# Optimization experiments

Measured on AMD Instinct MI355X. Metric: run time of the kernel, lower is better.

Reference implementation:

```python
import jax, jax.numpy as jnp
import numpy as np

B, S, D, F, A, H, O = 8, 2048, 64, 16, 32, 4, 64
HD = A // H  # head dim = 8
TWO_PI = 2.0 * np.pi


def setup_inputs() -> dict:
    key = jax.random.key(0)
    ks = jax.random.split(key, 10)
    sc = lambda k, sh, fan: (jax.random.normal(k, sh, jnp.float32) / np.sqrt(fan)).astype(jnp.float32)
    Din = D + 2 * D * F  # input width to gate/projection MLPs
    return dict(
        x=jax.random.normal(ks[0], (B, S, D), jnp.float32),
        freq_matrix=jnp.tile(jnp.linspace(1.0, 10.0, F, dtype=jnp.float32)[None, :], (D, 1)),
        phase=jax.random.normal(ks[1], (D, F), jnp.float32),
        freq_scale=jnp.ones((D, F), jnp.float32),
        Wq=sc(ks[2], (A, D), D), bq=jnp.zeros((A,), jnp.float32),          # query_proj
        Wk1=sc(ks[3], (A, 1), 1), bk1=jnp.zeros((A,), jnp.float32),        # key_proj (Linear(1, A))
        Wqi=sc(ks[4], (A, A), A), bqi=jnp.zeros((A,), jnp.float32),        # MHA in-proj (q slice)
        Wki=sc(ks[5], (A, A), A), bki=jnp.zeros((A,), jnp.float32),        # MHA in-proj (k slice)
        Wg=sc(ks[6], (O, Din), Din), bg=jnp.zeros((O,), jnp.float32),      # gate linear
        Wp=sc(ks[7], (O, Din), Din), bp=jnp.zeros((O,), jnp.float32),      # projection linear
    )


def reference(x, freq_matrix, phase, freq_scale, Wq, bq, Wk1, bk1, Wqi, bqi, Wki, bki, Wg, bg, Wp, bp):
    # x: [B, S, D]
    t = jnp.linspace(0.0, 1.0, S, dtype=x.dtype)                 # [S]
    f = freq_matrix * freq_scale                                 # [D, F]
    # fourier signal, batched over all input dims at once
    signal = TWO_PI * t[:, None, None] * f[None] + phase[None]   # [S, D, F]
    sin_f, cos_f = jnp.sin(signal), jnp.cos(signal)

    # MHA attention weights (averaged over heads) -- attn_out is discarded by the module
    queries = jnp.einsum('bsd,ad->bsa', x, Wq) + bq              # [B, S, A]
    q = (jnp.einsum('bsa,ea->bse', queries, Wqi) + bqi).reshape(B, S, H, HD)
    keys = f[:, :, None] * Wk1[None, None, :, 0] + bk1           # [D, F, A] via Linear(1, A)
    k = (jnp.einsum('dfa,ea->dfe', keys, Wki) + bki).reshape(D, F, H, HD)
    scores = jnp.einsum('bshe,dfhe->bdhsf', q, k) / np.sqrt(HD)  # [B, D, H, S, F]
    attn = jax.nn.softmax(scores, axis=-1).mean(axis=2)          # [B, D, S, F] (head-avg)
    aw = jnp.transpose(attn, (0, 2, 1, 3))                       # [B, S, D, F]

    # weighted fourier features; per-dim layout is [sin(F), cos(F)] to match torch cat order
    ff = jnp.concatenate([sin_f[None] * aw, cos_f[None] * aw], axis=-1)  # [B, S, D, 2F]
    ff = ff.reshape(B, S, D * 2 * F)

    ci = jnp.concatenate([x, ff], axis=-1)                       # [B, S, D + 2DF]
    gated = jax.nn.sigmoid(jnp.einsum('bsi,oi->bso', ci, Wg) + bg) * \
            jax.nn.silu(jnp.einsum('bsi,oi->bso', ci, Wp) + bp)
    return x + gated
```

## Files before the change

kernel.cpp:

```cpp
#include <hip/hip_runtime.h>
#include <math.h>

#define SS 2048
#define DIN 2112
#define NKT 66
#define TOK 32
#define NBLK 512
#define NTHR 512
#define ASTR 264
#define XSTR 68
#define CSTR 132
#define BFRAG_ELEMS (NKT * 8 * 64 * 8)
#define LOG2E 1.4426950408889634f
#define INV2PI 0.15915494309189535f

#define OFF_WP 135168
#define OFF_CP 135424
#define OFF_FV 135680
#define OFF_PH 136704
#define OFF_MX 137728

typedef __attribute__((ext_vector_type(4))) float f32x4;
typedef __attribute__((ext_vector_type(8))) short bf16x8;

__device__ __forceinline__ unsigned short f2bf(float x) {
    union { float f; unsigned u; } v; v.f = x;
    unsigned r = v.u + 0x7FFFu + ((v.u >> 16) & 1u);
    return (unsigned short)(r >> 16);
}
__device__ __forceinline__ unsigned pk2bf(float a, float b) {
    union { float f; unsigned u; } ua, ub; ua.f = a; ub.f = b;
    unsigned ra = ua.u + 0x7FFFu + ((ua.u >> 16) & 1u);
    unsigned rb = ub.u + 0x7FFFu + ((ub.u >> 16) & 1u);
#if __has_builtin(__builtin_amdgcn_perm)
    return __builtin_amdgcn_perm(rb, ra, 0x07060302u);
#else
    return (ra >> 16) | (rb & 0xFFFF0000u);
#endif
}

#if __has_builtin(__builtin_amdgcn_exp2f)
#define EXP2(x) __builtin_amdgcn_exp2f(x)
#else
#define EXP2(x) exp2f(x)
#endif
#if __has_builtin(__builtin_amdgcn_rcpf)
#define RCP(x) __builtin_amdgcn_rcpf(x)
#else
#define RCP(x) (1.0f / (x))
#endif
#if __has_builtin(__builtin_amdgcn_sinf)
#define SINR(x) __builtin_amdgcn_sinf(x)
#define COSR(x) __builtin_amdgcn_cosf(x)
#else
#define SINR(x) __sinf(6.283185307179586f * (x))
#define COSR(x) __cosf(6.283185307179586f * (x))
#endif

__global__ __launch_bounds__(256) void aff_pre(
    const float* __restrict__ Wq, const float* __restrict__ bq,
    const float* __restrict__ Wk1,
    const float* __restrict__ Wqi, const float* __restrict__ bqi,
    const float* __restrict__ Wki,
    const float* __restrict__ Wg, const float* __restrict__ Wp,
    const float* __restrict__ fm, const float* __restrict__ fs,
    const float* __restrict__ phase,
    float* __restrict__ ws)
{
    unsigned short* Bf = (unsigned short*)ws;
    const int tid = threadIdx.x;
    const int gid = blockIdx.x * 256 + tid;

    {
        int j  = gid & 7;
        int q  = (gid >> 3) & 3;
        int nl = (gid >> 5) & 15;
        int nt = (gid >> 9) & 7;
        int kt = gid >> 12;
        int k = kt * 32 + q * 8 + j;
        int n = nt * 16 + nl;
        float s = (n < 64) ? Wg[(size_t)n * DIN + k] : Wp[(size_t)(n - 64) * DIN + k];
        int dst = ((kt * 8 + nt) * 64 + q * 16 + nl) * 8 + j;
        Bf[dst] = f2bf(s);
    }

    if (blockIdx.x == 0) {
        float* WP = ws + OFF_WP;
        float* cP = ws + OFF_CP;
        float* fvg = ws + OFF_FV;
        float* phg = ws + OFF_PH;
        float* mxg = ws + OFF_MX;

        {
            float4 a = ((const float4*)fm)[tid];
            float4 b = ((const float4*)fs)[tid];
            float4 r; r.x = a.x * b.x; r.y = a.y * b.y; r.z = a.z * b.z; r.w = a.w * b.w;
            ((float4*)fvg)[tid] = r;
            float4 p = ((const float4*)phase)[tid];
            p.x *= INV2PI; p.y *= INV2PI; p.z *= INV2PI; p.w *= INV2PI;
            ((float4*)phg)[tid] = p;
        }
        if (tid < 64) {
            float mx = -1e30f, mn = 1e30f;
            #pragma unroll
            for (int f = 0; f < 16; ++f) {
                float v = fm[tid * 16 + f] * fs[tid * 16 + f];
                mx = fmaxf(mx, v); mn = fminf(mn, v);
            }
            mxg[tid * 2] = mx; mxg[tid * 2 + 1] = mn;
        }

        __shared__ float u[32];
        if (tid < 32) {
            float s = 0.f;
            #pragma unroll
            for (int a = 0; a < 32; ++a) s += Wki[tid * 32 + a] * Wk1[a];
            u[tid] = s;
        }
        __syncthreads();
        {
            const int h = tid >> 6;
            const int d = tid & 63;
            float s = 0.f;
            for (int j = 0; j < 8; ++j) {
                int e = h * 8 + j;
                float wc = 0.f;
                #pragma unroll
                for (int a = 0; a < 32; ++a) wc += Wqi[e * 32 + a] * Wq[a * 64 + d];
                s += u[e] * wc;
            }
            WP[h * 64 + d] = s * 0.35355339059327373f * LOG2E;
            if (d == 0) {
                float sc = 0.f;
                for (int j = 0; j < 8; ++j) {
                    int e = h * 8 + j;
                    float bcv = bqi[e];
                    #pragma unroll
                    for (int a = 0; a < 32; ++a) bcv += Wqi[e * 32 + a] * bq[a];
                    sc += u[e] * bcv;
                }
                cP[h] = sc * 0.35355339059327373f * LOG2E;
            }
        }
    }
}

__global__ __launch_bounds__(NTHR, 6) void aff_main(
    const float* __restrict__ x,
    const float* __restrict__ ws_c,
    const float* __restrict__ bg, const float* __restrict__ bp,
    float* __restrict__ out)
{
    __shared__ __align__(16) float xs[TOK * XSTR];
    __shared__ __align__(16) unsigned short Ab[2][TOK * ASTR];
    __shared__ __align__(16) float Pl[TOK * 4];
    __shared__ __align__(16) float fvs[1024];
    __shared__ __align__(16) float phl[1024];
    __shared__ __align__(16) float mxs[128];

    const unsigned short* Bfu = (const unsigned short*)ws_c;
    const bf16x8* Bv = (const bf16x8*)Bfu;
    const float* WP  = ws_c + OFF_WP;
    const float* cP  = ws_c + OFF_CP;
    const float* fvg = ws_c + OFF_FV;
    const float* phg = ws_c + OFF_PH;
    const float* mxg = ws_c + OFF_MX;

    const int tid  = threadIdx.x;
    const int lane = tid & 63;
    const int w    = tid >> 6;
    const int t0   = blockIdx.x * TOK;
    const int lm   = lane & 15;
    const int lq   = lane >> 4;
    const int fh   = lq & 1;
    const int dsel = lane >> 5;
    const int dloc = ((w & 3) << 1) + dsel;
    const int tb   = ((w >> 2) << 4) + lm;

    if (tid < 256) {
        ((float4*)fvs)[tid] = ((const float4*)fvg)[tid];
        if (tid < 32) ((float4*)mxs)[tid] = ((const float4*)mxg)[tid];
    } else {
        ((float4*)phl)[tid - 256] = ((const float4*)phg)[tid - 256];
    }
    {
        int t = tid >> 4, j4 = (tid & 15) * 4;
        float4 xv = *(const float4*)(x + (size_t)(t0 + t) * 64 + j4);
        *(float4*)(xs + t * XSTR + j4) = xv;
    }
    __syncthreads();

    if (tid < 128) {
        int t = tid & 31, h = tid >> 5;
        float acc = cP[h];
        const float* wp = WP + h * 64;
        #pragma unroll 8
        for (int d = 0; d < 64; ++d) acc = fmaf(wp[d], xs[t * XSTR + d], acc);
        Pl[t * 4 + h] = acc;
    }

    f32x4 acc0 = {}, acc1 = {};

    #pragma unroll
    for (int ks = 0; ks < 2; ++ks) {
        bf16x8 b = Bv[((size_t)ks * 8 + w) * 64 + lane];
        #pragma unroll
        for (int mt = 0; mt < 2; ++mt) {
            const float* xr = xs + (mt * 16 + lm) * XSTR + ks * 32 + lq * 8;
            float4 fa = *(const float4*)xr;
            float4 fb = *(const float4*)(xr + 4);
            union { unsigned u[4]; bf16x8 v; } av;
            av.u[0] = pk2bf(fa.x, fa.y); av.u[1] = pk2bf(fa.z, fa.w);
            av.u[2] = pk2bf(fb.x, fb.y); av.u[3] = pk2bf(fb.z, fb.w);
            if (mt == 0) acc0 = __builtin_amdgcn_mfma_f32_16x16x32_bf16(av.v, b, acc0, 0, 0, 0);
            else         acc1 = __builtin_amdgcn_mfma_f32_16x16x32_bf16(av.v, b, acc1, 0, 0, 0);
        }
    }
    __syncthreads();

    const float w2 = (float)((t0 + tb) & (SS - 1)) * (1.0f / 2047.0f);

    auto build = [&](int ch, int buf) {
        const int d = ch * 8 + dloc;
        const float4 fA = *(const float4*)(fvs + d * 16 + fh * 8);
        const float4 fB = *(const float4*)(fvs + d * 16 + fh * 8 + 4);
        const float4 pA = *(const float4*)(phl + d * 16 + fh * 8);
        const float4 pB = *(const float4*)(phl + d * 16 + fh * 8 + 4);
        const float4 Pv = *(const float4*)(Pl + tb * 4);
        const float mxv = mxs[d * 2], mnv = mxs[d * 2 + 1];
        float fl[8] = {fA.x, fA.y, fA.z, fA.w, fB.x, fB.y, fB.z, fB.w};
        float pr[8] = {pA.x, pA.y, pA.z, pA.w, pB.x, pB.y, pB.z, pB.w};
        float aw[8] = {0.f, 0.f, 0.f, 0.f, 0.f, 0.f, 0.f, 0.f};
        float Ph4[4] = {Pv.x, Pv.y, Pv.z, Pv.w};
        #pragma unroll
        for (int h = 0; h < 4; ++h) {
            float Ph = Ph4[h];
            float m = fmaxf(mxv * Ph, mnv * Ph);
            float e[8]; float s = 0.f;
            #pragma unroll
            for (int j = 0; j < 8; ++j) { e[j] = EXP2(fmaf(fl[j], Ph, -m)); s += e[j]; }
            float z = s + __shfl_xor(s, 16);
            float inv = 0.25f * RCP(z);
            #pragma unroll
            for (int j = 0; j < 8; ++j) aw[j] = fmaf(e[j], inv, aw[j]);
        }
        unsigned sv[4], cv[4];
        #pragma unroll
        for (int jp = 0; jp < 4; ++jp) {
            int j0 = 2 * jp;
            float X0 = fmaf(w2, fl[j0], pr[j0]);
            float X1 = fmaf(w2, fl[j0 + 1], pr[j0 + 1]);
            float a0 = aw[j0], a1 = aw[j0 + 1];
            sv[jp] = pk2bf(a0 * SINR(X0), a1 * SINR(X1));
            cv[jp] = pk2bf(a0 * COSR(X0), a1 * COSR(X1));
        }
        unsigned short* dst = &Ab[buf][tb * ASTR + dloc * 32 + fh * 8];
        uint4 v0; v0.x = sv[0]; v0.y = sv[1]; v0.z = sv[2]; v0.w = sv[3];
        uint4 v1; v1.x = cv[0]; v1.y = cv[1]; v1.z = cv[2]; v1.w = cv[3];
        *(uint4*)dst = v0;
        *(uint4*)(dst + 16) = v1;
    };

    build(0, 0);
    __syncthreads();

    for (int ch = 0; ch < 8; ++ch) {
        const unsigned short* Ar = &Ab[ch & 1][0];
        #pragma unroll
        for (int ks = 0; ks < 8; ++ks) {
            const size_t kt = (size_t)(2 + ch * 8 + ks);
            bf16x8 b  = Bv[(kt * 8 + w) * 64 + lane];
            bf16x8 a0 = *(const bf16x8*)(Ar + lm * ASTR + ks * 32 + lq * 8);
            bf16x8 a1 = *(const bf16x8*)(Ar + (16 + lm) * ASTR + ks * 32 + lq * 8);
            acc0 = __builtin_amdgcn_mfma_f32_16x16x32_bf16(a0, b, acc0, 0, 0, 0);
            acc1 = __builtin_amdgcn_mfma_f32_16x16x32_bf16(a1, b, acc1, 0, 0, 0);
        }
        if (ch < 7) build(ch + 1, (ch + 1) & 1);
        __syncthreads();
    }

    float* Cb = (float*)(&Ab[0][0]);
    #pragma unroll
    for (int r = 0; r < 4; ++r) {
        Cb[(lq * 4 + r) * CSTR + w * 16 + lm]        = acc0[r];
        Cb[(16 + lq * 4 + r) * CSTR + w * 16 + lm]   = acc1[r];
    }
    __syncthreads();
    {
        int t = tid >> 4, o0 = (tid & 15) * 4;
        float4 g4 = *(float4*)(Cb + t * CSTR + o0);
        float4 p4 = *(float4*)(Cb + t * CSTR + 64 + o0);
        float4 bg4 = *(const float4*)(bg + o0);
        float4 bp4 = *(const float4*)(bp + o0);
        float4 xr = *(float4*)(xs + t * XSTR + o0);
        float4 o;
        { float g = g4.x + bg4.x, p = p4.x + bp4.x;
          float sg = RCP(1.f + EXP2(-g * LOG2E));
          float sp = RCP(1.f + EXP2(-p * LOG2E));
          o.x = fmaf(p * sg, sp, xr.x); }
        { float g = g4.y + bg4.y, p = p4.y + bp4.y;
          float sg = RCP(1.f + EXP2(-g * LOG2E));
          float sp = RCP(1.f + EXP2(-p * LOG2E));
          o.y = fmaf(p * sg, sp, xr.y); }
        { float g = g4.z + bg4.z, p = p4.z + bp4.z;
          float sg = RCP(1.f + EXP2(-g * LOG2E));
          float sp = RCP(1.f + EXP2(-p * LOG2E));
          o.z = fmaf(p * sg, sp, xr.z); }
        { float g = g4.w + bg4.w, p = p4.w + bp4.w;
          float sg = RCP(1.f + EXP2(-g * LOG2E));
          float sp = RCP(1.f + EXP2(-p * LOG2E));
          o.w = fmaf(p * sg, sp, xr.w); }
        *(float4*)(out + (size_t)(t0 + t) * 64 + o0) = o;
    }
}

extern "C" void kernel_launch(void* const* d_in, const int* in_sizes, int n_in,
                              void* d_out, int out_size, void* d_ws, size_t ws_size,
                              hipStream_t stream) {
    (void)in_sizes; (void)n_in; (void)out_size; (void)ws_size;
    const float* x    = (const float*)d_in[0];
    const float* fm   = (const float*)d_in[1];
    const float* phs  = (const float*)d_in[2];
    const float* fs   = (const float*)d_in[3];
    const float* Wq   = (const float*)d_in[4];
    const float* bq   = (const float*)d_in[5];
    const float* Wk1  = (const float*)d_in[6];
    const float* Wqi  = (const float*)d_in[8];
    const float* bqi  = (const float*)d_in[9];
    const float* Wki  = (const float*)d_in[10];
    const float* Wg   = (const float*)d_in[12];
    const float* bg   = (const float*)d_in[13];
    const float* Wp   = (const float*)d_in[14];
    const float* bp   = (const float*)d_in[15];
    float* out = (float*)d_out;
    float* ws  = (float*)d_ws;

    aff_pre<<<BFRAG_ELEMS / 256, 256, 0, stream>>>(Wq, bq, Wk1, Wqi, bqi, Wki, Wg, Wp,
                                                   fm, fs, phs, ws);
    aff_main<<<NBLK, NTHR, 0, stream>>>(x, (const float*)ws, bg, bp, out);
}
```

Measured before the change: 123.5 us.

## Halve token tile to 16 with 256 threads and switch MFMA operands to fp16

```diff
diff --git a/kernel.cpp b/kernel.cpp
--- a/kernel.cpp
+++ b/kernel.cpp
@@ -4,9 +4,9 @@
 #define SS 2048
 #define DIN 2112
 #define NKT 66
-#define TOK 32
-#define NBLK 512
-#define NTHR 512
+#define TOK 16
+#define NBLK 1024
+#define NTHR 256
 #define ASTR 264
 #define XSTR 68
 #define CSTR 132
@@ -21,21 +21,18 @@
 #define OFF_MX 137728
 
 typedef __attribute__((ext_vector_type(4))) float f32x4;
-typedef __attribute__((ext_vector_type(8))) short bf16x8;
-
-__device__ __forceinline__ unsigned short f2bf(float x) {
-    union { float f; unsigned u; } v; v.f = x;
-    unsigned r = v.u + 0x7FFFu + ((v.u >> 16) & 1u);
-    return (unsigned short)(r >> 16);
-}
-__device__ __forceinline__ unsigned pk2bf(float a, float b) {
-    union { float f; unsigned u; } ua, ub; ua.f = a; ub.f = b;
-    unsigned ra = ua.u + 0x7FFFu + ((ua.u >> 16) & 1u);
-    unsigned rb = ub.u + 0x7FFFu + ((ub.u >> 16) & 1u);
-#if __has_builtin(__builtin_amdgcn_perm)
-    return __builtin_amdgcn_perm(rb, ra, 0x07060302u);
+typedef __attribute__((ext_vector_type(8))) _Float16 f16x8;
+typedef __attribute__((ext_vector_type(2))) __fp16 fp16v2;
+
+__device__ __forceinline__ unsigned pkh(float a, float b) {
+#if __has_builtin(__builtin_amdgcn_cvt_pkrtz)
+    union { fp16v2 h; unsigned u; } r;
+    r.h = __builtin_amdgcn_cvt_pkrtz(a, b);
+    return r.u;
 #else
-    return (ra >> 16) | (rb & 0xFFFF0000u);
+    union { _Float16 h[2]; unsigned u; } r;
+    r.h[0] = (_Float16)a; r.h[1] = (_Float16)b;
+    return r.u;
 #endif
 }
 
@@ -67,7 +64,7 @@
     const float* __restrict__ phase,
     float* __restrict__ ws)
 {
-    unsigned short* Bf = (unsigned short*)ws;
+    _Float16* Bf = (_Float16*)ws;
     const int tid = threadIdx.x;
     const int gid = blockIdx.x * 256 + tid;
 
@@ -81,7 +78,7 @@
         int n = nt * 16 + nl;
         float s = (n < 64) ? Wg[(size_t)n * DIN + k] : Wp[(size_t)(n - 64) * DIN + k];
         int dst = ((kt * 8 + nt) * 64 + q * 16 + nl) * 8 + j;
-        Bf[dst] = f2bf(s);
+        Bf[dst] = (_Float16)s;
     }
 
     if (blockIdx.x == 0) {
@@ -145,21 +142,20 @@
     }
 }
 
-__global__ __launch_bounds__(NTHR, 6) void aff_main(
+__global__ __launch_bounds__(NTHR, 4) void aff_main(
     const float* __restrict__ x,
     const float* __restrict__ ws_c,
     const float* __restrict__ bg, const float* __restrict__ bp,
     float* __restrict__ out)
 {
     __shared__ __align__(16) float xs[TOK * XSTR];
-    __shared__ __align__(16) unsigned short Ab[2][TOK * ASTR];
+    __shared__ __align__(16) _Float16 Ab[2][TOK * ASTR];
     __shared__ __align__(16) float Pl[TOK * 4];
     __shared__ __align__(16) float fvs[1024];
     __shared__ __align__(16) float phl[1024];
     __shared__ __align__(16) float mxs[128];
 
-    const unsigned short* Bfu = (const unsigned short*)ws_c;
-    const bf16x8* Bv = (const bf16x8*)Bfu;
+    const f16x8* Bv = (const f16x8*)ws_c;
     const float* WP  = ws_c + OFF_WP;
     const float* cP  = ws_c + OFF_CP;
     const float* fvg = ws_c + OFF_FV;
@@ -174,15 +170,11 @@
     const int lq   = lane >> 4;
     const int fh   = lq & 1;
     const int dsel = lane >> 5;
-    const int dloc = ((w & 3) << 1) + dsel;
-    const int tb   = ((w >> 2) << 4) + lm;
-
-    if (tid < 256) {
-        ((float4*)fvs)[tid] = ((const float4*)fvg)[tid];
-        if (tid < 32) ((float4*)mxs)[tid] = ((const float4*)mxg)[tid];
-    } else {
-        ((float4*)phl)[tid - 256] = ((const float4*)phg)[tid - 256];
-    }
+    const int dloc = (w << 1) + dsel;
+
+    ((float4*)fvs)[tid] = ((const float4*)fvg)[tid];
+    ((float4*)phl)[tid] = ((const float4*)phg)[tid];
+    if (tid < 32) ((float4*)mxs)[tid] = ((const float4*)mxg)[tid];
     {
         int t = tid >> 4, j4 = (tid & 15) * 4;
         float4 xv = *(const float4*)(x + (size_t)(t0 + t) * 64 + j4);
@@ -191,43 +183,50 @@
     __syncthreads();
 
     if (tid < 128) {
-        int t = tid & 31, h = tid >> 5;
-        float acc = cP[h];
-        const float* wp = WP + h * 64;
+        int t = tid & 15, dh = (tid >> 4) & 1, h = tid >> 5;
+        float acc = 0.f;
+        const float* wp = WP + h * 64 + dh * 32;
+        const float* xr = xs + t * XSTR + dh * 32;
         #pragma unroll 8
-        for (int d = 0; d < 64; ++d) acc = fmaf(wp[d], xs[t * XSTR + d], acc);
-        Pl[t * 4 + h] = acc;
+        for (int d = 0; d < 32; ++d) acc = fmaf(wp[d], xr[d], acc);
+        acc += __shfl_xor(acc, 16);
+        if (dh == 0) Pl[t * 4 + h] = acc + cP[h];
     }
 
     f32x4 acc0 = {}, acc1 = {};
 
     #pragma unroll
     for (int ks = 0; ks < 2; ++ks) {
-        bf16x8 b = Bv[((size_t)ks * 8 + w) * 64 + lane];
-        #pragma unroll
-        for (int mt = 0; mt < 2; ++mt) {
-            const float* xr = xs + (mt * 16 + lm) * XSTR + ks * 32 + lq * 8;
-            float4 fa = *(const float4*)xr;
-            float4 fb = *(const float4*)(xr + 4);
-            union { unsigned u[4]; bf16x8 v; } av;
-            av.u[0] = pk2bf(fa.x, fa.y); av.u[1] = pk2bf(fa.z, fa.w);
-            av.u[2] = pk2bf(fb.x, fb.y); av.u[3] = pk2bf(fb.z, fb.w);
-            if (mt == 0) acc0 = __builtin_amdgcn_mfma_f32_16x16x32_bf16(av.v, b, acc0, 0, 0, 0);
-            else         acc1 = __builtin_amdgcn_mfma_f32_16x16x32_bf16(av.v, b, acc1, 0, 0, 0);
-        }
+        f16x8 b0 = Bv[((size_t)ks * 8 + 2 * w) * 64 + lane];
+        f16x8 b1 = Bv[((size_t)ks * 8 + 2 * w + 1) * 64 + lane];
+        const float* xr = xs + lm * XSTR + ks * 32 + lq * 8;
+        float4 fa = *(const float4*)xr;
+        float4 fb = *(const float4*)(xr + 4);
+        union { unsigned u[4]; f16x8 v; } av;
+        av.u[0] = pkh(fa.x, fa.y); av.u[1] = pkh(fa.z, fa.w);
+        av.u[2] = pkh(fb.x, fb.y); av.u[3] = pkh(fb.z, fb.w);
+        acc0 = __builtin_amdgcn_mfma_f32_16x16x32_f16(av.v, b0, acc0, 0, 0, 0);
+        acc1 = __builtin_amdgcn_mfma_f32_16x16x32_f16(av.v, b1, acc1, 0, 0, 0);
     }
     __syncthreads();
 
-    const float w2 = (float)((t0 + tb) & (SS - 1)) * (1.0f / 2047.0f);
-
-    auto build = [&](int ch, int buf) {
-        const int d = ch * 8 + dloc;
-        const float4 fA = *(const float4*)(fvs + d * 16 + fh * 8);
-        const float4 fB = *(const float4*)(fvs + d * 16 + fh * 8 + 4);
-        const float4 pA = *(const float4*)(phl + d * 16 + fh * 8);
-        const float4 pB = *(const float4*)(phl + d * 16 + fh * 8 + 4);
-        const float4 Pv = *(const float4*)(Pl + tb * 4);
-        const float mxv = mxs[d * 2], mnv = mxs[d * 2 + 1];
+    const float w2 = (float)((t0 + lm) & (SS - 1)) * (1.0f / 2047.0f);
+
+    const float* fvp0 = fvs + dloc * 16 + fh * 8;
+    const float* php0 = phl + dloc * 16 + fh * 8;
+    const float* mxp0 = mxs + dloc * 2;
+    _Float16* dst0 = &Ab[0][lm * ASTR + dloc * 32 + fh * 8];
+    _Float16* dst1 = &Ab[1][lm * ASTR + dloc * 32 + fh * 8];
+
+    auto build = [&](int ch, _Float16* dst) {
+        const float* fvp = fvp0 + ch * 128;
+        const float* php = php0 + ch * 128;
+        const float4 fA = *(const float4*)fvp;
+        const float4 fB = *(const float4*)(fvp + 4);
+        const float4 pA = *(const float4*)php;
+        const float4 pB = *(const float4*)(php + 4);
+        const float4 Pv = *(const float4*)(Pl + lm * 4);
+        const float mxv = mxp0[ch * 16], mnv = mxp0[ch * 16 + 1];
         float fl[8] = {fA.x, fA.y, fA.z, fA.w, fB.x, fB.y, fB.z, fB.w};
         float pr[8] = {pA.x, pA.y, pA.z, pA.w, pB.x, pB.y, pB.z, pB.w};
         float aw[8] = {0.f, 0.f, 0.f, 0.f, 0.f, 0.f, 0.f, 0.f};
@@ -251,39 +250,38 @@
             float X0 = fmaf(w2, fl[j0], pr[j0]);
             float X1 = fmaf(w2, fl[j0 + 1], pr[j0 + 1]);
             float a0 = aw[j0], a1 = aw[j0 + 1];
-            sv[jp] = pk2bf(a0 * SINR(X0), a1 * SINR(X1));
-            cv[jp] = pk2bf(a0 * COSR(X0), a1 * COSR(X1));
-        }
-        unsigned short* dst = &Ab[buf][tb * ASTR + dloc * 32 + fh * 8];
+            sv[jp] = pkh(a0 * SINR(X0), a1 * SINR(X1));
+            cv[jp] = pkh(a0 * COSR(X0), a1 * COSR(X1));
+        }
         uint4 v0; v0.x = sv[0]; v0.y = sv[1]; v0.z = sv[2]; v0.w = sv[3];
         uint4 v1; v1.x = cv[0]; v1.y = cv[1]; v1.z = cv[2]; v1.w = cv[3];
         *(uint4*)dst = v0;
         *(uint4*)(dst + 16) = v1;
     };
 
-    build(0, 0);
+    build(0, dst0);
     __syncthreads();
 
     for (int ch = 0; ch < 8; ++ch) {
-        const unsigned short* Ar = &Ab[ch & 1][0];
+        const _Float16* Ar = &Ab[ch & 1][0];
         #pragma unroll
         for (int ks = 0; ks < 8; ++ks) {
             const size_t kt = (size_t)(2 + ch * 8 + ks);
-            bf16x8 b  = Bv[(kt * 8 + w) * 64 + lane];
-            bf16x8 a0 = *(const bf16x8*)(Ar + lm * ASTR + ks * 32 + lq * 8);
-            bf16x8 a1 = *(const bf16x8*)(Ar + (16 + lm) * ASTR + ks * 32 + lq * 8);
-            acc0 = __builtin_amdgcn_mfma_f32_16x16x32_bf16(a0, b, acc0, 0, 0, 0);
-            acc1 = __builtin_amdgcn_mfma_f32_16x16x32_bf16(a1, b, acc1, 0, 0, 0);
-        }
-        if (ch < 7) build(ch + 1, (ch + 1) & 1);
+            f16x8 b0 = Bv[(kt * 8 + 2 * w) * 64 + lane];
+            f16x8 b1 = Bv[(kt * 8 + 2 * w + 1) * 64 + lane];
+            f16x8 a = *(const f16x8*)(Ar + lm * ASTR + ks * 32 + lq * 8);
+            acc0 = __builtin_amdgcn_mfma_f32_16x16x32_f16(a, b0, acc0, 0, 0, 0);
+            acc1 = __builtin_amdgcn_mfma_f32_16x16x32_f16(a, b1, acc1, 0, 0, 0);
+        }
+        if (ch < 7) build(ch + 1, (ch & 1) ? dst0 : dst1);
         __syncthreads();
     }
 
     float* Cb = (float*)(&Ab[0][0]);
     #pragma unroll
     for (int r = 0; r < 4; ++r) {
-        Cb[(lq * 4 + r) * CSTR + w * 16 + lm]        = acc0[r];
-        Cb[(16 + lq * 4 + r) * CSTR + w * 16 + lm]   = acc1[r];
+        Cb[(lq * 4 + r) * CSTR + (2 * w) * 16 + lm]     = acc0[r];
+        Cb[(lq * 4 + r) * CSTR + (2 * w + 1) * 16 + lm] = acc1[r];
     }
     __syncthreads();
     {
```

Result: faster. 119.6 us (-3.2%).
